# Kernel tuning notes

Measured on AMD Instinct MI355X. Metric: run time of the kernel, lower is better.

Reference implementation:

```python
import jax, jax.numpy as jnp
import numpy as np

N = 30000      # nodes
E = 480000     # edges (before self loops)
C = 64         # in_channels
L = 32         # latent_dim
H = 2          # heads
SLOPE = 0.2    # PyG GATConv default negative_slope


def _param(key, shape, fan_in):
    return jax.random.normal(key, shape, jnp.float32) * (1.0 / np.sqrt(fan_in))


def setup_inputs() -> dict:
    key = jax.random.key(0)
    ks = jax.random.split(key, 32)
    d = {
        "x": jax.random.normal(ks[0], (N, C), jnp.float32),
        "edge_index": jax.random.randint(ks[1], (2, E), 0, N),
        "use_neighbors": 1,
        # GATConv params: W [heads*out, in], att_src/att_dst [heads, out], bias [heads*out]
        # encoder_conv1: in=C, out=2C, heads=H
        "W1": _param(ks[2], (H * 2 * C, C), C),
        "as1": _param(ks[3], (H, 2 * C), 2 * C),
        "ad1": _param(ks[4], (H, 2 * C), 2 * C),
        "b1": jnp.zeros((H * 2 * C,), jnp.float32),
        # encoder_conv2: in=2C*H, out=L, heads=1
        "W2": _param(ks[5], (L, 2 * C * H), 2 * C * H),
        "as2": _param(ks[6], (1, L), L),
        "ad2": _param(ks[7], (1, L), L),
        "b2": jnp.zeros((L,), jnp.float32),
        # decoder_conv1: in=L, out=2C, heads=H
        "W3": _param(ks[8], (H * 2 * C, L), L),
        "as3": _param(ks[9], (H, 2 * C), 2 * C),
        "ad3": _param(ks[10], (H, 2 * C), 2 * C),
        "b3": jnp.zeros((H * 2 * C,), jnp.float32),
        # decoder_conv2: in=2C*H, out=C, heads=1
        "W4": _param(ks[11], (C, 2 * C * H), 2 * C * H),
        "as4": _param(ks[12], (1, C), C),
        "ad4": _param(ks[13], (1, C), C),
        "b4": jnp.zeros((C,), jnp.float32),
        # dense (non-neighbor) branch Linear params [out, in] + bias
        "el1w": _param(ks[14], (2 * C, C), C), "el1b": jnp.zeros((2 * C,), jnp.float32),
        "el2w": _param(ks[15], (L, 2 * C), 2 * C), "el2b": jnp.zeros((L,), jnp.float32),
        "dl1w": _param(ks[16], (2 * C, L), L), "dl1b": jnp.zeros((2 * C,), jnp.float32),
        "dl2w": _param(ks[17], (C, 2 * C), 2 * C), "dl2b": jnp.zeros((C,), jnp.float32),
    }
    return d


def gat_conv(x, src, dst, W, att_src, att_dst, bias, heads, out_ch):
    """PyG GATConv (concat=True, self loops already in src/dst)."""
    n = x.shape[0]
    h = (x @ W.T).reshape(n, heads, out_ch)            # [N,H,F]
    a_s = jnp.sum(h * att_src[None], -1)               # [N,H]
    a_d = jnp.sum(h * att_dst[None], -1)               # [N,H]
    e = jax.nn.leaky_relu(a_s[src] + a_d[dst], SLOPE)  # [Etot,H]
    m = jax.ops.segment_max(e, dst, num_segments=n)
    ex = jnp.exp(e - m[dst])
    den = jax.ops.segment_sum(ex, dst, num_segments=n)
    alpha = ex / den[dst]                              # segment softmax over incoming edges
    msg = h[src] * alpha[..., None]                    # [Etot,H,F]
    out = jax.ops.segment_sum(msg, dst, num_segments=n)
    return out.reshape(n, heads * out_ch) + bias


def reference(x, edge_index, use_neighbors,
              W1, as1, ad1, b1, W2, as2, ad2, b2,
              W3, as3, ad3, b3, W4, as4, ad4, b4,
              el1w, el1b, el2w, el2b, dl1w, dl1b, dl2w, dl2b):
    if use_neighbors:
        loops = jnp.arange(N)
        src = jnp.concatenate([edge_index[0], loops])
        dst = jnp.concatenate([edge_index[1], loops])
        h = jax.nn.relu(gat_conv(x, src, dst, W1, as1, ad1, b1, H, 2 * C))
        z = gat_conv(h, src, dst, W2, as2, ad2, b2, 1, L)
        h = jax.nn.relu(gat_conv(z, src, dst, W3, as3, ad3, b3, H, 2 * C))
        return gat_conv(h, src, dst, W4, as4, ad4, b4, 1, C)
    else:
        h = jax.nn.relu(x @ el1w.T + el1b)
        z = h @ el2w.T + el2b
        h = jax.nn.relu(z @ dl1w.T + dl1b)
        return h @ dl2w.T + dl2b
```

## Files before the change

### kernel.cpp

```cpp
#include <hip/hip_runtime.h>
#include <hip/hip_bf16.h>
#include <math.h>

#define NODES 30000
#define WAVE 64
#define SCAN_T 1024
#define SCAN_CH 32
#define SCAN_CAP (SCAN_T * SCAN_CH)

static __device__ __forceinline__ float lrelu(float x) {
    return (x > 0.f) ? x : 0.2f * x;
}

__global__ __launch_bounds__(256) void gemm_xwt(
    const float* __restrict__ X, int lda, const float* __restrict__ W,
    const float* __restrict__ bias, float* __restrict__ out, int ldc,
    int Nrows, int M, int K, int relu,
    const int* __restrict__ flag, int wantFlag)
{
    if (((*flag != 0) ? 1 : 0) != wantFlag) return;

    const int z = blockIdx.z;
    X += (size_t)z * K;
    W += (size_t)z * M * K;
    if (bias) bias += (size_t)z * M;
    out += (size_t)z * M;

    __shared__ float As[16][68];
    __shared__ float Bs[16][68];

    const int t  = threadIdx.x;
    const int tx = t & 15;
    const int ty = t >> 4;
    const int rowBase = blockIdx.y * 64;
    const int colBase = blockIdx.x * 64;

    float acc[4][4];
#pragma unroll
    for (int i = 0; i < 4; i++)
#pragma unroll
        for (int j = 0; j < 4; j++) acc[i][j] = 0.f;

    const int r_ld = t >> 2;
    const int k_ld = (t & 3) * 4;

    for (int kt = 0; kt < K; kt += 16) {
        float4 av = make_float4(0.f, 0.f, 0.f, 0.f);
        int grow = rowBase + r_ld;
        if (grow < Nrows)
            av = *reinterpret_cast<const float4*>(&X[(size_t)grow * lda + kt + k_ld]);
        As[k_ld + 0][r_ld] = av.x;
        As[k_ld + 1][r_ld] = av.y;
        As[k_ld + 2][r_ld] = av.z;
        As[k_ld + 3][r_ld] = av.w;
        float4 bv = make_float4(0.f, 0.f, 0.f, 0.f);
        int gm = colBase + r_ld;
        if (gm < M)
            bv = *reinterpret_cast<const float4*>(&W[(size_t)gm * K + kt + k_ld]);
        Bs[k_ld + 0][r_ld] = bv.x;
        Bs[k_ld + 1][r_ld] = bv.y;
        Bs[k_ld + 2][r_ld] = bv.z;
        Bs[k_ld + 3][r_ld] = bv.w;
        __syncthreads();

#pragma unroll
        for (int kk = 0; kk < 16; ++kk) {
            const float4 a = *reinterpret_cast<const float4*>(&As[kk][ty * 4]);
            const float4 b = *reinterpret_cast<const float4*>(&Bs[kk][tx * 4]);
            acc[0][0] += a.x * b.x; acc[0][1] += a.x * b.y; acc[0][2] += a.x * b.z; acc[0][3] += a.x * b.w;
            acc[1][0] += a.y * b.x; acc[1][1] += a.y * b.y; acc[1][2] += a.y * b.z; acc[1][3] += a.y * b.w;
            acc[2][0] += a.z * b.x; acc[2][1] += a.z * b.y; acc[2][2] += a.z * b.z; acc[2][3] += a.z * b.w;
            acc[3][0] += a.w * b.x; acc[3][1] += a.w * b.y; acc[3][2] += a.w * b.z; acc[3][3] += a.w * b.w;
        }
        __syncthreads();
    }

#pragma unroll
    for (int i = 0; i < 4; i++) {
        int row = rowBase + ty * 4 + i;
        if (row >= Nrows) continue;
        int col0 = colBase + tx * 4;
        if (col0 >= M) continue;
        float4 v = make_float4(acc[i][0], acc[i][1], acc[i][2], acc[i][3]);
        if (bias) {
            v.x += bias[col0 + 0]; v.y += bias[col0 + 1];
            v.z += bias[col0 + 2]; v.w += bias[col0 + 3];
        }
        if (relu) {
            v.x = fmaxf(v.x, 0.f); v.y = fmaxf(v.y, 0.f);
            v.z = fmaxf(v.z, 0.f); v.w = fmaxf(v.w, 0.f);
        }
        *reinterpret_cast<float4*>(&out[(size_t)row * ldc + col0]) = v;
    }
}

template <int HH, int F, int K>
__global__ __launch_bounds__(256) void fold_att(
    const float* __restrict__ W, const float* __restrict__ as_,
    const float* __restrict__ ad_, float* __restrict__ us,
    float* __restrict__ ud, const int* __restrict__ flag)
{
    if (*flag == 0) return;
    const int b   = blockIdx.x;
    const int sel = b / HH;
    const int h   = b % HH;
    const float* att = sel ? ad_ : as_;
    float* uo = sel ? ud : us;

    constexpr int NG = 256 / K;
    const int k  = threadIdx.x % K;
    const int fg = threadIdx.x / K;

    float s = 0.f;
#pragma unroll
    for (int f = fg; f < F; f += NG)
        s += att[h * F + f] * W[(size_t)(h * F + f) * K + k];

    __shared__ float red[256];
    red[threadIdx.x] = s;
    __syncthreads();
    if (fg == 0) {
        float tot = s;
#pragma unroll
        for (int g = 1; g < NG; g++) tot += red[g * K + k];
        uo[h * K + k] = tot;
    }
}

template <int K, int HH>
__global__ __launch_bounds__(256) void att_from_x(
    const float* __restrict__ xin, const float* __restrict__ us,
    const float* __restrict__ ud, float* __restrict__ as_out,
    float* __restrict__ ad_out, const int* __restrict__ flag)
{
    if (*flag == 0) return;
    constexpr int NPW = WAVE / K;
    const int wid  = threadIdx.x >> 6;
    const int lane = threadIdx.x & 63;
    const int sub  = lane / K;
    const int col  = lane % K;
    const int node = (blockIdx.x * 4 + wid) * NPW + sub;

    float v = 0.f;
    if (node < NODES) v = xin[(size_t)node * K + col];
    float ps[HH], pd[HH];
#pragma unroll
    for (int h = 0; h < HH; h++) {
        ps[h] = v * us[h * K + col];
        pd[h] = v * ud[h * K + col];
    }
#pragma unroll
    for (int off = K / 2; off; off >>= 1) {
#pragma unroll
        for (int h = 0; h < HH; h++) {
            ps[h] += __shfl_xor(ps[h], off);
            pd[h] += __shfl_xor(pd[h], off);
        }
    }
    if (col == 0 && node < NODES) {
#pragma unroll
        for (int h = 0; h < HH; h++) {
            as_out[node * HH + h] = ps[h];
            ad_out[node * HH + h] = pd[h];
        }
    }
}

template <int HH>
__global__ void gather_e(const float* __restrict__ as_, const int* __restrict__ csr_src,
                         float* __restrict__ eb, int Etot, const int* __restrict__ flag)
{
    if (*flag == 0) return;
    int i = blockIdx.x * blockDim.x + threadIdx.x;
    if (i >= Etot) return;
    int s = csr_src[i];
    if (HH == 1) {
        eb[i] = as_[s];
    } else {
        float2 v = *reinterpret_cast<const float2*>(&as_[s * 2]);
        *reinterpret_cast<float2*>(&eb[(size_t)i * 2]) = v;
    }
}

template <int K, int HH>
__global__ __launch_bounds__(256) void gat_aggr_x(
    const float* __restrict__ xin, const float* __restrict__ eb,
    const float* __restrict__ ad_, const int* __restrict__ rowptr,
    const int* __restrict__ csr_src, float* __restrict__ agg,
    const int* __restrict__ flag)
{
    if (*flag == 0) return;
    const int node = blockIdx.x * 4 + (threadIdx.x >> 6);
    const int lane = threadIdx.x & 63;
    if (node >= NODES) return;

    const int beg = rowptr[node], end = rowptr[node + 1];

    float adv[HH], mx[HH], den[HH];
#pragma unroll
    for (int h = 0; h < HH; h++) {
        adv[h] = ad_[node * HH + h];
        mx[h]  = -1e30f;
        den[h] = 0.f;
    }
    for (int i = beg + lane; i < end; i += WAVE) {
#pragma unroll
        for (int h = 0; h < HH; h++)
            mx[h] = fmaxf(mx[h], lrelu(eb[(size_t)i * HH + h] + adv[h]));
    }
#pragma unroll
    for (int h = 0; h < HH; h++)
#pragma unroll
        for (int off = 32; off; off >>= 1)
            mx[h] = fmaxf(mx[h], __shfl_xor(mx[h], off));
    for (int i = beg + lane; i < end; i += WAVE) {
#pragma unroll
        for (int h = 0; h < HH; h++)
            den[h] += __expf(lrelu(eb[(size_t)i * HH + h] + adv[h]) - mx[h]);
    }
#pragma unroll
    for (int h = 0; h < HH; h++)
#pragma unroll
        for (int off = 32; off; off >>= 1)
            den[h] += __shfl_xor(den[h], off);
    float rden[HH];
#pragma unroll
    for (int h = 0; h < HH; h++) rden[h] = 1.f / den[h];

    constexpr int LPG = K / 4;
    constexpr int GR  = WAVE / LPG;
    const int esub = lane / LPG;
    const int c4   = lane % LPG;

    float4 acc[HH];
#pragma unroll
    for (int h = 0; h < HH; h++) acc[h] = make_float4(0.f, 0.f, 0.f, 0.f);

    for (int i = beg + esub; i < end; i += GR) {
        int s = csr_src[i];
        float w[HH];
#pragma unroll
        for (int h = 0; h < HH; h++)
            w[h] = __expf(lrelu(eb[(size_t)i * HH + h] + adv[h]) - mx[h]);
        float4 xv = *reinterpret_cast<const float4*>(&xin[(size_t)s * K + c4 * 4]);
#pragma unroll
        for (int h = 0; h < HH; h++) {
            acc[h].x += xv.x * w[h];
            acc[h].y += xv.y * w[h];
            acc[h].z += xv.z * w[h];
            acc[h].w += xv.w * w[h];
        }
    }
#pragma unroll
    for (int off = LPG; off < WAVE; off <<= 1) {
#pragma unroll
        for (int h = 0; h < HH; h++) {
            acc[h].x += __shfl_xor(acc[h].x, off);
            acc[h].y += __shfl_xor(acc[h].y, off);
            acc[h].z += __shfl_xor(acc[h].z, off);
            acc[h].w += __shfl_xor(acc[h].w, off);
        }
    }
    if (esub == 0) {
#pragma unroll
        for (int h = 0; h < HH; h++) {
            float4 o = make_float4(acc[h].x * rden[h], acc[h].y * rden[h],
                                   acc[h].z * rden[h], acc[h].w * rden[h]);
            *reinterpret_cast<float4*>(&agg[(size_t)node * (HH * K) + h * K + c4 * 4]) = o;
        }
    }
}

template <int HF, int RELU>
__global__ __launch_bounds__(256) void gat_aggr_h(
    const float* __restrict__ hsrc, const float* __restrict__ eb,
    const float* __restrict__ ad_, const int* __restrict__ rowptr,
    const int* __restrict__ csr_src, const float* __restrict__ bias,
    float* __restrict__ out, const int* __restrict__ flag)
{
    if (*flag == 0) return;
    const int node = blockIdx.x * 4 + (threadIdx.x >> 6);
    const int lane = threadIdx.x & 63;
    if (node >= NODES) return;

    const int beg = rowptr[node], end = rowptr[node + 1];
    const float adv = ad_[node];

    float mx = -1e30f, den = 0.f;
    for (int i = beg + lane; i < end; i += WAVE)
        mx = fmaxf(mx, lrelu(eb[i] + adv));
#pragma unroll
    for (int off = 32; off; off >>= 1)
        mx = fmaxf(mx, __shfl_xor(mx, off));
    for (int i = beg + lane; i < end; i += WAVE)
        den += __expf(lrelu(eb[i] + adv) - mx);
#pragma unroll
    for (int off = 32; off; off >>= 1)
        den += __shfl_xor(den, off);
    const float rden = 1.f / den;

    constexpr int LPG = HF / 4;
    constexpr int GR  = WAVE / LPG;
    const int esub = lane / LPG;
    const int c4   = lane % LPG;

    float4 acc = make_float4(0.f, 0.f, 0.f, 0.f);
    for (int i = beg + esub; i < end; i += GR) {
        int s = csr_src[i];
        float w = __expf(lrelu(eb[i] + adv) - mx);
        float4 hv = *reinterpret_cast<const float4*>(&hsrc[(size_t)s * HF + c4 * 4]);
        acc.x += hv.x * w; acc.y += hv.y * w; acc.z += hv.z * w; acc.w += hv.w * w;
    }
#pragma unroll
    for (int off = LPG; off < WAVE; off <<= 1) {
        acc.x += __shfl_xor(acc.x, off);
        acc.y += __shfl_xor(acc.y, off);
        acc.z += __shfl_xor(acc.z, off);
        acc.w += __shfl_xor(acc.w, off);
    }
    if (esub == 0) {
        float4 bv = *reinterpret_cast<const float4*>(&bias[c4 * 4]);
        float4 o = make_float4(acc.x * rden + bv.x, acc.y * rden + bv.y,
                               acc.z * rden + bv.z, acc.w * rden + bv.w);
        if (RELU) {
            o.x = fmaxf(o.x, 0.f); o.y = fmaxf(o.y, 0.f);
            o.z = fmaxf(o.z, 0.f); o.w = fmaxf(o.w, 0.f);
        }
        *reinterpret_cast<float4*>(&out[(size_t)node * HF + c4 * 4]) = o;
    }
}

__global__ void zero_int(int* __restrict__ p, int n, const int* __restrict__ flag)
{
    if (*flag == 0) return;
    for (int i = blockIdx.x * blockDim.x + threadIdx.x; i < n; i += gridDim.x * blockDim.x)
        p[i] = 0;
}

__global__ void count_deg(const int* __restrict__ ei, int* __restrict__ deg,
                          int E_, int Nn, const int* __restrict__ flag)
{
    if (*flag == 0) return;
    int e = blockIdx.x * blockDim.x + threadIdx.x;
    int tot = E_ + Nn;
    if (e >= tot) return;
    int dst = (e < E_) ? ei[E_ + e] : (e - E_);
    atomicAdd(&deg[dst], 1);
}

__global__ __launch_bounds__(SCAN_T) void scan_deg(
    const int* __restrict__ deg, int* __restrict__ rowptr,
    int* __restrict__ cursor, const int* __restrict__ flag)
{
    if (*flag == 0) return;
    __shared__ int sums[SCAN_T];
    const int t = threadIdx.x;
    const int base = t * SCAN_CH;

    int v[SCAN_CH];
    const int4* dp = reinterpret_cast<const int4*>(deg + base);
#pragma unroll
    for (int j = 0; j < SCAN_CH / 4; j++) {
        int4 q = dp[j];
        v[4 * j + 0] = q.x; v[4 * j + 1] = q.y;
        v[4 * j + 2] = q.z; v[4 * j + 3] = q.w;
    }
    int s = 0;
#pragma unroll
    for (int j = 0; j < SCAN_CH; j++) s += v[j];
    sums[t] = s;
    __syncthreads();
    for (int off = 1; off < SCAN_T; off <<= 1) {
        int x = (t >= off) ? sums[t - off] : 0;
        __syncthreads();
        sums[t] += x;
        __syncthreads();
    }
    int run = sums[t] - s;
    if (t == 0) rowptr[0] = 0;
#pragma unroll
    for (int j = 0; j < SCAN_CH; j++) {
        cursor[base + j] = run;
        run += v[j];
        rowptr[base + j + 1] = run;
    }
}

__global__ void scatter_edges(const int* __restrict__ ei, int* __restrict__ cursor,
                              int* __restrict__ csr_src, int E_, int Nn,
                              const int* __restrict__ flag)
{
    if (*flag == 0) return;
    int e = blockIdx.x * blockDim.x + threadIdx.x;
    int tot = E_ + Nn;
    if (e >= tot) return;
    int src, dst;
    if (e < E_) { src = ei[e]; dst = ei[E_ + e]; }
    else        { src = e - E_; dst = src; }
    int pos = atomicAdd(&cursor[dst], 1);
    csr_src[pos] = src;
}

extern "C" void kernel_launch(void* const* d_in, const int* in_sizes, int n_in,
                              void* d_out, int out_size, void* d_ws, size_t ws_size,
                              hipStream_t stream)
{
    const float* x    = (const float*)d_in[0];
    const int*   ei   = (const int*)d_in[1];
    const int*   flag = (const int*)d_in[2];
    const float* W1 = (const float*)d_in[3];
    const float* as1 = (const float*)d_in[4];
    const float* ad1 = (const float*)d_in[5];
    const float* b1 = (const float*)d_in[6];
    const float* W2 = (const float*)d_in[7];
    const float* as2 = (const float*)d_in[8];
    const float* ad2 = (const float*)d_in[9];
    const float* b2 = (const float*)d_in[10];
    const float* W3 = (const float*)d_in[11];
    const float* as3 = (const float*)d_in[12];
    const float* ad3 = (const float*)d_in[13];
    const float* b3 = (const float*)d_in[14];
    const float* W4 = (const float*)d_in[15];
    const float* as4 = (const float*)d_in[16];
    const float* ad4 = (const float*)d_in[17];
    const float* b4 = (const float*)d_in[18];
    const float* el1w = (const float*)d_in[19];
    const float* el1b = (const float*)d_in[20];
    const float* el2w = (const float*)d_in[21];
    const float* el2b = (const float*)d_in[22];
    const float* dl1w = (const float*)d_in[23];
    const float* dl1b = (const float*)d_in[24];
    const float* dl2w = (const float*)d_in[25];
    const float* dl2b = (const float*)d_in[26];

    const int E_   = in_sizes[1] / 2;
    const int Etot = E_ + NODES;

    char* base = (char*)d_ws;
    size_t off = 0;
    auto carve = [&](size_t bytes) -> void* {
        void* p = base + off;
        off = (off + bytes + 255) & ~(size_t)255;
        return p;
    };
    float* T0  = (float*)carve((size_t)NODES * 128 * 4);
    float* A   = (float*)carve((size_t)NODES * 256 * 4);
    float* T1  = (float*)carve((size_t)NODES * 64 * 4);
    float* Bz  = (float*)carve((size_t)NODES * 32 * 4);
    float* asb = (float*)carve((size_t)NODES * 2 * 4);
    float* adb = (float*)carve((size_t)NODES * 2 * 4);
    float* eb  = (float*)carve((size_t)Etot * 2 * 4);
    float* u1s = (float*)carve(2 * 64 * 4);
    float* u1d = (float*)carve(2 * 64 * 4);
    float* u3s = (float*)carve(2 * 32 * 4);
    float* u3d = (float*)carve(2 * 32 * 4);
    int* deg    = (int*)carve((size_t)SCAN_CAP * 4);
    int* rowptr = (int*)carve((size_t)(SCAN_CAP + 1) * 4);
    int* cursor = (int*)carve((size_t)SCAN_CAP * 4);
    int* csr    = (int*)carve((size_t)Etot * 4);
    (void)ws_size; (void)n_in; (void)out_size;

    float* outp = (float*)d_out;
    float* agg  = T0;

    const int nodeBlocks = (NODES + 3) / 4;
    const int edgeBlocks = (Etot + 255) / 256;
    dim3 blk(256);
    const int rowTiles = (NODES + 63) / 64;

    zero_int<<<(SCAN_CAP + 255) / 256, 256, 0, stream>>>(deg, SCAN_CAP, flag);
    count_deg<<<edgeBlocks, 256, 0, stream>>>(ei, deg, E_, NODES, flag);
    scan_deg<<<1, SCAN_T, 0, stream>>>(deg, rowptr, cursor, flag);
    scatter_edges<<<edgeBlocks, 256, 0, stream>>>(ei, cursor, csr, E_, NODES, flag);

    fold_att<2, 128, 64><<<4, 256, 0, stream>>>(W1, as1, ad1, u1s, u1d, flag);
    att_from_x<64, 2><<<nodeBlocks, blk, 0, stream>>>(x, u1s, u1d, asb, adb, flag);
    gather_e<2><<<edgeBlocks, 256, 0, stream>>>(asb, csr, eb, Etot, flag);
    gat_aggr_x<64, 2><<<nodeBlocks, blk, 0, stream>>>(x, eb, adb, rowptr, csr, agg, flag);
    gemm_xwt<<<dim3(2, rowTiles, 2), blk, 0, stream>>>(agg, 128, W1, b1, A, 256, NODES, 128, 64, 1, flag, 1);

    gemm_xwt<<<dim3(1, rowTiles, 1), blk, 0, stream>>>(A, 256, W2, nullptr, T1, 32, NODES, 32, 256, 0, flag, 1);
    att_from_x<32, 1><<<(NODES + 7) / 8, blk, 0, stream>>>(T1, as2, ad2, asb, adb, flag);
    gather_e<1><<<edgeBlocks, 256, 0, stream>>>(asb, csr, eb, Etot, flag);
    gat_aggr_h<32, 0><<<nodeBlocks, blk, 0, stream>>>(T1, eb, adb, rowptr, csr, b2, Bz, flag);

    fold_att<2, 128, 32><<<4, 256, 0, stream>>>(W3, as3, ad3, u3s, u3d, flag);
    att_from_x<32, 2><<<(NODES + 7) / 8, blk, 0, stream>>>(Bz, u3s, u3d, asb, adb, flag);
    gather_e<2><<<edgeBlocks, 256, 0, stream>>>(asb, csr, eb, Etot, flag);
    gat_aggr_x<32, 2><<<nodeBlocks, blk, 0, stream>>>(Bz, eb, adb, rowptr, csr, agg, flag);
    gemm_xwt<<<dim3(2, rowTiles, 2), blk, 0, stream>>>(agg, 64, W3, b3, A, 256, NODES, 128, 32, 1, flag, 1);

    gemm_xwt<<<dim3(1, rowTiles, 1), blk, 0, stream>>>(A, 256, W4, nullptr, T1, 64, NODES, 64, 256, 0, flag, 1);
    att_from_x<64, 1><<<nodeBlocks, blk, 0, stream>>>(T1, as4, ad4, asb, adb, flag);
    gather_e<1><<<edgeBlocks, 256, 0, stream>>>(asb, csr, eb, Etot, flag);
    gat_aggr_h<64, 0><<<nodeBlocks, blk, 0, stream>>>(T1, eb, adb, rowptr, csr, b4, outp, flag);

    gemm_xwt<<<dim3(2, rowTiles, 1), blk, 0, stream>>>(x,  64,  el1w, el1b, T0,   128, NODES, 128, 64, 1, flag, 0);
    gemm_xwt<<<dim3(1, rowTiles, 1), blk, 0, stream>>>(T0, 128, el2w, el2b, Bz,   32,  NODES, 32, 128, 0, flag, 0);
    gemm_xwt<<<dim3(2, rowTiles, 1), blk, 0, stream>>>(Bz, 32,  dl1w, dl1b, A,    128, NODES, 128, 32, 1, flag, 0);
    gemm_xwt<<<dim3(1, rowTiles, 1), blk, 0, stream>>>(A,  128, dl2w, dl2b, outp, 64,  NODES, 64, 128, 0, flag, 0);
}
```

Before: 401.2 us.

## Drop per-edge gather kernels, fuse attention dots into GEMM, single-pass softmax for small degrees

Removes the four gather_e kernels and the per-edge eb buffer. The aggregation kernels now read per-node attention scores indirectly through csr_src. For heads=1 layers, the attention dot products are folded into the GEMM epilogue with a 16-lane shuffle reduction, which removes two att_from_x launches. For nodes with degree up to 64, the aggregation kernels compute logits once per lane and broadcast the weights by shuffle instead of recomputing exp across three passes. The cost is an extra indirection per edge and more code paths; the GEMM fusion relies on one block covering the full output width (M ≤ 64).

Result: faster. 383.3 us (-4.5%).

```diff
diff --git a/kernel.cpp b/kernel.cpp
--- a/kernel.cpp
+++ b/kernel.cpp
@@ -16,6 +16,8 @@
     const float* __restrict__ X, int lda, const float* __restrict__ W,
     const float* __restrict__ bias, float* __restrict__ out, int ldc,
     int Nrows, int M, int K, int relu,
+    const float* __restrict__ att_s, const float* __restrict__ att_d,
+    float* __restrict__ as_out, float* __restrict__ ad_out,
     const int* __restrict__ flag, int wantFlag)
 {
     if (((*flag != 0) ? 1 : 0) != wantFlag) return;
@@ -75,11 +77,11 @@
         __syncthreads();
     }
 
+    const int col0 = colBase + tx * 4;
 #pragma unroll
     for (int i = 0; i < 4; i++) {
         int row = rowBase + ty * 4 + i;
         if (row >= Nrows) continue;
-        int col0 = colBase + tx * 4;
         if (col0 >= M) continue;
         float4 v = make_float4(acc[i][0], acc[i][1], acc[i][2], acc[i][3]);
         if (bias) {
@@ -91,6 +93,29 @@
             v.z = fmaxf(v.z, 0.f); v.w = fmaxf(v.w, 0.f);
         }
         *reinterpret_cast<float4*>(&out[(size_t)row * ldc + col0]) = v;
+    }
+
+    if (att_s) {
+        float4 asv = make_float4(0.f, 0.f, 0.f, 0.f), adv = asv;
+        if (col0 < M) {
+            asv = *reinterpret_cast<const float4*>(&att_s[col0]);
+            adv = *reinterpret_cast<const float4*>(&att_d[col0]);
+        }
+#pragma unroll
+        for (int i = 0; i < 4; i++) {
+            float ps = acc[i][0] * asv.x + acc[i][1] * asv.y + acc[i][2] * asv.z + acc[i][3] * asv.w;
+            float pd = acc[i][0] * adv.x + acc[i][1] * adv.y + acc[i][2] * adv.z + acc[i][3] * adv.w;
+#pragma unroll
+            for (int off = 8; off; off >>= 1) {
+                ps += __shfl_xor(ps, off);
+                pd += __shfl_xor(pd, off);
+            }
+            int row = rowBase + ty * 4 + i;
+            if (tx == 0 && row < Nrows) {
+                as_out[row] = ps;
+                ad_out[row] = pd;
+            }
+        }
     }
 }
 
@@ -166,25 +191,9 @@
     }
 }
 
-template <int HH>
-__global__ void gather_e(const float* __restrict__ as_, const int* __restrict__ csr_src,
-                         float* __restrict__ eb, int Etot, const int* __restrict__ flag)
-{
-    if (*flag == 0) return;
-    int i = blockIdx.x * blockDim.x + threadIdx.x;
-    if (i >= Etot) return;
-    int s = csr_src[i];
-    if (HH == 1) {
-        eb[i] = as_[s];
-    } else {
-        float2 v = *reinterpret_cast<const float2*>(&as_[s * 2]);
-        *reinterpret_cast<float2*>(&eb[(size_t)i * 2]) = v;
-    }
-}
-
 template <int K, int HH>
 __global__ __launch_bounds__(256) void gat_aggr_x(
-    const float* __restrict__ xin, const float* __restrict__ eb,
+    const float* __restrict__ xin, const float* __restrict__ as_,
     const float* __restrict__ ad_, const int* __restrict__ rowptr,
     const int* __restrict__ csr_src, float* __restrict__ agg,
     const int* __restrict__ flag)
@@ -195,37 +204,71 @@
     if (node >= NODES) return;
 
     const int beg = rowptr[node], end = rowptr[node + 1];
-
-    float adv[HH], mx[HH], den[HH];
-#pragma unroll
-    for (int h = 0; h < HH; h++) {
-        adv[h] = ad_[node * HH + h];
-        mx[h]  = -1e30f;
-        den[h] = 0.f;
-    }
-    for (int i = beg + lane; i < end; i += WAVE) {
+    const int deg = end - beg;
+
+    float adv[HH];
+#pragma unroll
+    for (int h = 0; h < HH; h++) adv[h] = ad_[node * HH + h];
+
+    float wl[HH];
+    float mx[HH], rden[HH];
+    const bool fast = (deg <= WAVE);
+
+    if (fast) {
+        float e[HH];
+        int i = beg + lane;
+        if (i < end) {
+            int s = csr_src[i];
+#pragma unroll
+            for (int h = 0; h < HH; h++)
+                e[h] = lrelu(as_[s * HH + h] + adv[h]);
+        } else {
+#pragma unroll
+            for (int h = 0; h < HH; h++) e[h] = -1e30f;
+        }
+#pragma unroll
+        for (int h = 0; h < HH; h++) {
+            mx[h] = e[h];
+#pragma unroll
+            for (int off = 32; off; off >>= 1)
+                mx[h] = fmaxf(mx[h], __shfl_xor(mx[h], off));
+            float ex = __expf(e[h] - mx[h]);
+            wl[h] = ex;
+            float dn = ex;
+#pragma unroll
+            for (int off = 32; off; off >>= 1)
+                dn += __shfl_xor(dn, off);
+            rden[h] = 1.f / dn;
+        }
+    } else {
+        float den[HH];
+#pragma unroll
+        for (int h = 0; h < HH; h++) { mx[h] = -1e30f; den[h] = 0.f; }
+        for (int i = beg + lane; i < end; i += WAVE) {
+            int s = csr_src[i];
+#pragma unroll
+            for (int h = 0; h < HH; h++)
+                mx[h] = fmaxf(mx[h], lrelu(as_[s * HH + h] + adv[h]));
+        }
 #pragma unroll
         for (int h = 0; h < HH; h++)
-            mx[h] = fmaxf(mx[h], lrelu(eb[(size_t)i * HH + h] + adv[h]));
-    }
-#pragma unroll
-    for (int h = 0; h < HH; h++)
-#pragma unroll
-        for (int off = 32; off; off >>= 1)
-            mx[h] = fmaxf(mx[h], __shfl_xor(mx[h], off));
-    for (int i = beg + lane; i < end; i += WAVE) {
-#pragma unroll
-        for (int h = 0; h < HH; h++)
-            den[h] += __expf(lrelu(eb[(size_t)i * HH + h] + adv[h]) - mx[h]);
-    }
-#pragma unroll
-    for (int h = 0; h < HH; h++)
-#pragma unroll
-        for (int off = 32; off; off >>= 1)
-            den[h] += __shfl_xor(den[h], off);
-    float rden[HH];
-#pragma unroll
-    for (int h = 0; h < HH; h++) rden[h] = 1.f / den[h];
+#pragma unroll
+            for (int off = 32; off; off >>= 1)
+                mx[h] = fmaxf(mx[h], __shfl_xor(mx[h], off));
+        for (int i = beg + lane; i < end; i += WAVE) {
+            int s = csr_src[i];
+#pragma unroll
+            for (int h = 0; h < HH; h++)
+                den[h] += __expf(lrelu(as_[s * HH + h] + adv[h]) - mx[h]);
+        }
+#pragma unroll
+        for (int h = 0; h < HH; h++) {
+#pragma unroll
+            for (int off = 32; off; off >>= 1)
+                den[h] += __shfl_xor(den[h], off);
+            rden[h] = 1.f / den[h];
+        }
+    }
 
     constexpr int LPG = K / 4;
     constexpr int GR  = WAVE / LPG;
@@ -236,19 +279,43 @@
 #pragma unroll
     for (int h = 0; h < HH; h++) acc[h] = make_float4(0.f, 0.f, 0.f, 0.f);
 
-    for (int i = beg + esub; i < end; i += GR) {
-        int s = csr_src[i];
-        float w[HH];
-#pragma unroll
-        for (int h = 0; h < HH; h++)
-            w[h] = __expf(lrelu(eb[(size_t)i * HH + h] + adv[h]) - mx[h]);
-        float4 xv = *reinterpret_cast<const float4*>(&xin[(size_t)s * K + c4 * 4]);
-#pragma unroll
-        for (int h = 0; h < HH; h++) {
-            acc[h].x += xv.x * w[h];
-            acc[h].y += xv.y * w[h];
-            acc[h].z += xv.z * w[h];
-            acc[h].w += xv.w * w[h];
+    if (fast) {
+        const int iters = (deg + GR - 1) / GR;
+        for (int it = 0; it < iters; ++it) {
+            const int i = beg + it * GR + esub;
+            const bool valid = (i < end);
+            const int srcl = valid ? (i - beg) : 0;
+            float w[HH];
+#pragma unroll
+            for (int h = 0; h < HH; h++)
+                w[h] = __shfl(wl[h], srcl);
+            if (valid) {
+                int s = csr_src[i];
+                float4 xv = *reinterpret_cast<const float4*>(&xin[(size_t)s * K + c4 * 4]);
+#pragma unroll
+                for (int h = 0; h < HH; h++) {
+                    acc[h].x += xv.x * w[h];
+                    acc[h].y += xv.y * w[h];
+                    acc[h].z += xv.z * w[h];
+                    acc[h].w += xv.w * w[h];
+                }
+            }
+        }
+    } else {
+        for (int i = beg + esub; i < end; i += GR) {
+            int s = csr_src[i];
+            float w[HH];
+#pragma unroll
+            for (int h = 0; h < HH; h++)
+                w[h] = __expf(lrelu(as_[s * HH + h] + adv[h]) - mx[h]);
+            float4 xv = *reinterpret_cast<const float4*>(&xin[(size_t)s * K + c4 * 4]);
+#pragma unroll
+            for (int h = 0; h < HH; h++) {
+                acc[h].x += xv.x * w[h];
+                acc[h].y += xv.y * w[h];
+                acc[h].z += xv.z * w[h];
+                acc[h].w += xv.w * w[h];
+            }
         }
     }
 #pragma unroll
@@ -273,7 +340,7 @@
 
 template <int HF, int RELU>
 __global__ __launch_bounds__(256) void gat_aggr_h(
-    const float* __restrict__ hsrc, const float* __restrict__ eb,
+    const float* __restrict__ hsrc, const float* __restrict__ as_,
     const float* __restrict__ ad_, const int* __restrict__ rowptr,
     const int* __restrict__ csr_src, const float* __restrict__ bias,
     float* __restrict__ out, const int* __restrict__ flag)
@@ -284,20 +351,49 @@
     if (node >= NODES) return;
 
     const int beg = rowptr[node], end = rowptr[node + 1];
+    const int deg = end - beg;
     const float adv = ad_[node];
 
-    float mx = -1e30f, den = 0.f;
-    for (int i = beg + lane; i < end; i += WAVE)
-        mx = fmaxf(mx, lrelu(eb[i] + adv));
-#pragma unroll
-    for (int off = 32; off; off >>= 1)
-        mx = fmaxf(mx, __shfl_xor(mx, off));
-    for (int i = beg + lane; i < end; i += WAVE)
-        den += __expf(lrelu(eb[i] + adv) - mx);
-#pragma unroll
-    for (int off = 32; off; off >>= 1)
-        den += __shfl_xor(den, off);
-    const float rden = 1.f / den;
+    float wl, mx, rden;
+    const bool fast = (deg <= WAVE);
+
+    if (fast) {
+        int i = beg + lane;
+        float e = -1e30f;
+        if (i < end) {
+            int s = csr_src[i];
+            e = lrelu(as_[s] + adv);
+        }
+        mx = e;
+#pragma unroll
+        for (int off = 32; off; off >>= 1)
+            mx = fmaxf(mx, __shfl_xor(mx, off));
+        wl = __expf(e - mx);
+        float dn = wl;
+#pragma unroll
+        for (int off = 32; off; off >>= 1)
+            dn += __shfl_xor(dn, off);
+        rden = 1.f / dn;
+    } else {
+        mx = -1e30f;
+        float den = 0.f;
+        for (int i = beg + lane; i < end; i += WAVE) {
+            int s = csr_src[i];
+            mx = fmaxf(mx, lrelu(as_[s] + adv));
+        }
+#pragma unroll
+        for (int off = 32; off; off >>= 1)
+            mx = fmaxf(mx, __shfl_xor(mx, off));
+        for (int i = beg + lane; i < end; i += WAVE) {
+            int s = csr_src[i];
+            den += __expf(lrelu(as_[s] + adv) - mx);
+        }
+#pragma unroll
+        for (int off = 32; off; off >>= 1)
+            den += __shfl_xor(den, off);
+        rden = 1.f / den;
+        wl = 0.f;
+    }
 
     constexpr int LPG = HF / 4;
     constexpr int GR  = WAVE / LPG;
@@ -305,11 +401,26 @@
     const int c4   = lane % LPG;
 
     float4 acc = make_float4(0.f, 0.f, 0.f, 0.f);
-    for (int i = beg + esub; i < end; i += GR) {
-        int s = csr_src[i];
-        float w = __expf(lrelu(eb[i] + adv) - mx);
-        float4 hv = *reinterpret_cast<const float4*>(&hsrc[(size_t)s * HF + c4 * 4]);
-        acc.x += hv.x * w; acc.y += hv.y * w; acc.z += hv.z * w; acc.w += hv.w * w;
+    if (fast) {
+        const int iters = (deg + GR - 1) / GR;
+        for (int it = 0; it < iters; ++it) {
+            const int i = beg + it * GR + esub;
+            const bool valid = (i < end);
+            const int srcl = valid ? (i - beg) : 0;
+            float w = __shfl(wl, srcl);
+            if (valid) {
+                int s = csr_src[i];
+                float4 hv = *reinterpret_cast<const float4*>(&hsrc[(size_t)s * HF + c4 * 4]);
+                acc.x += hv.x * w; acc.y += hv.y * w; acc.z += hv.z * w; acc.w += hv.w * w;
+            }
+        }
+    } else {
+        for (int i = beg + esub; i < end; i += GR) {
+            int s = csr_src[i];
+            float w = __expf(lrelu(as_[s] + adv) - mx);
+            float4 hv = *reinterpret_cast<const float4*>(&hsrc[(size_t)s * HF + c4 * 4]);
+            acc.x += hv.x * w; acc.y += hv.y * w; acc.z += hv.z * w; acc.w += hv.w * w;
+        }
     }
 #pragma unroll
     for (int off = LPG; off < WAVE; off <<= 1) {
@@ -449,7 +560,6 @@
     float* Bz  = (float*)carve((size_t)NODES * 32 * 4);
     float* asb = (float*)carve((size_t)NODES * 2 * 4);
     float* adb = (float*)carve((size_t)NODES * 2 * 4);
-    float* eb  = (float*)carve((size_t)Etot * 2 * 4);
     float* u1s = (float*)carve(2 * 64 * 4);
     float* u1d = (float*)carve(2 * 64 * 4);
     float* u3s = (float*)carve(2 * 32 * 4);
@@ -475,28 +585,30 @@
 
     fold_att<2, 128, 64><<<4, 256, 0, stream>>>(W1, as1, ad1, u1s, u1d, flag);
     att_from_x<64, 2><<<nodeBlocks, blk, 0, stream>>>(x, u1s, u1d, asb, adb, flag);
-    gather_e<2><<<edgeBlocks, 256, 0, stream>>>(asb, csr, eb, Etot, flag);
-    gat_aggr_x<64, 2><<<nodeBlocks, blk, 0, stream>>>(x, eb, adb, rowptr, csr, agg, flag);
-    gemm_xwt<<<dim3(2, rowTiles, 2), blk, 0, stream>>>(agg, 128, W1, b1, A, 256, NODES, 128, 64, 1, flag, 1);
-
-    gemm_xwt<<<dim3(1, rowTiles, 1), blk, 0, stream>>>(A, 256, W2, nullptr, T1, 32, NODES, 32, 256, 0, flag, 1);
-    att_from_x<32, 1><<<(NODES + 7) / 8, blk, 0, stream>>>(T1, as2, ad2, asb, adb, flag);
-    gather_e<1><<<edgeBlocks, 256, 0, stream>>>(asb, csr, eb, Etot, flag);
-    gat_aggr_h<32, 0><<<nodeBlocks, blk, 0, stream>>>(T1, eb, adb, rowptr, csr, b2, Bz, flag);
+    gat_aggr_x<64, 2><<<nodeBlocks, blk, 0, stream>>>(x, asb, adb, rowptr, csr, agg, flag);
+    gemm_xwt<<<dim3(2, rowTiles, 2), blk, 0, stream>>>(agg, 128, W1, b1, A, 256, NODES, 128, 64, 1,
+                                                       nullptr, nullptr, nullptr, nullptr, flag, 1);
+
+    gemm_xwt<<<dim3(1, rowTiles, 1), blk, 0, stream>>>(A, 256, W2, nullptr, T1, 32, NODES, 32, 256, 0,
+                                                       as2, ad2, asb, adb, flag, 1);
+    gat_aggr_h<32, 0><<<nodeBlocks, blk, 0, stream>>>(T1, asb, adb, rowptr, csr, b2, Bz, flag);
 
     fold_att<2, 128, 32><<<4, 256, 0, stream>>>(W3, as3, ad3, u3s, u3d, flag);
     att_from_x<32, 2><<<(NODES + 7) / 8, blk, 0, stream>>>(Bz, u3s, u3d, asb, adb, flag);
-    gather_e<2><<<edgeBlocks, 256, 0, stream>>>(asb, csr, eb, Etot, flag);
-    gat_aggr_x<32, 2><<<nodeBlocks, blk, 0, stream>>>(Bz, eb, adb, rowptr, csr, agg, flag);
-    gemm_xwt<<<dim3(2, rowTiles, 2), blk, 0, stream>>>(agg, 64, W3, b3, A, 256, NODES, 128, 32, 1, flag, 1);
-
-    gemm_xwt<<<dim3(1, rowTiles, 1), blk, 0, stream>>>(A, 256, W4, nullptr, T1, 64, NODES, 64, 256, 0, flag, 1);
-    att_from_x<64, 1><<<nodeBlocks, blk, 0, stream>>>(T1, as4, ad4, asb, adb, flag);
-    gather_e<1><<<edgeBlocks, 256, 0, stream>>>(asb, csr, eb, Etot, flag);
-    gat_aggr_h<64, 0><<<nodeBlocks, blk, 0, stream>>>(T1, eb, adb, rowptr, csr, b4, outp, flag);
-
-    gemm_xwt<<<dim3(2, rowTiles, 1), blk, 0, stream>>>(x,  64,  el1w, el1b, T0,   128, NODES, 128, 64, 1, flag, 0);
-    gemm_xwt<<<dim3(1, rowTiles, 1), blk, 0, stream>>>(T0, 128, el2w, el2b, Bz,   32,  NODES, 32, 128, 0, flag, 0);
-    gemm_xwt<<<dim3(2, rowTiles, 1), blk, 0, stream>>>(Bz, 32,  dl1w, dl1b, A,    128, NODES, 128, 32, 1, flag, 0);
-    gemm_xwt<<<dim3(1, rowTiles, 1), blk, 0, stream>>>(A,  128, dl2w, dl2b, outp, 64,  NODES, 64, 128, 0, flag, 0);
-}
+    gat_aggr_x<32, 2><<<nodeBlocks, blk, 0, stream>>>(Bz, asb, adb, rowptr, csr, agg, flag);
+    gemm_xwt<<<dim3(2, rowTiles, 2), blk, 0, stream>>>(agg, 64, W3, b3, A, 256, NODES, 128, 32, 1,
+                                                       nullptr, nullptr, nullptr, nullptr, flag, 1);
+
+    gemm_xwt<<<dim3(1, rowTiles, 1), blk, 0, stream>>>(A, 256, W4, nullptr, T1, 64, NODES, 64, 256, 0,
+                                                       as4, ad4, asb, adb, flag, 1);
+    gat_aggr_h<64, 0><<<nodeBlocks, blk, 0, stream>>>(T1, asb, adb, rowptr, csr, b4, outp, flag);
+
+    gemm_xwt<<<dim3(2, rowTiles, 1), blk, 0, stream>>>(x,  64,  el1w, el1b, T0,   128, NODES, 128, 64, 1,
+                                                       nullptr, nullptr, nullptr, nullptr, flag, 0);
+    gemm_xwt<<<dim3(1, rowTiles, 1), blk, 0, stream>>>(T0, 128, el2w, el2b, Bz,   32,  NODES, 32, 128, 0,
+                                                       nullptr, nullptr, nullptr, nullptr, flag, 0);
+    gemm_xwt<<<dim3(2, rowTiles, 1), blk, 0, stream>>>(Bz, 32,  dl1w, dl1b, A,    128, NODES, 128, 32, 1,
+                                                       nullptr, nullptr, nullptr, nullptr, flag, 0);
+    gemm_xwt<<<dim3(1, rowTiles, 1), blk, 0, stream>>>(A,  128, dl2w, dl2b, outp, 64,  NODES, 64, 128, 0,
+                                                       nullptr, nullptr, nullptr, nullptr, flag, 0);
+}
```
